# Kernel tuning notes

Hardware: AMD Instinct MI355X
Metric: run time of the kernel (lower is better)

## Reference

```python
import jax, jax.numpy as jnp
import numpy as np

NUM_LAYERS = 2
D_MODEL = 512
NHEAD = 8
SEQ_LEN = 2048
WINDOW = 64
D_FF = 4 * D_MODEL
LN_EPS = 1e-5


def _log_sparse_allowed(seq_len, window_size):
    # True where attention is allowed: causal local window + log2-strided lookback.
    allowed = np.zeros((seq_len, seq_len), dtype=bool)
    for i in range(seq_len):
        allowed[i, max(0, i - window_size): i + 1] = True
        for j in range(int(np.log2(i + 1)) + 1):
            step = 2 ** j
            if i - step >= 0:
                allowed[i, i - step] = True
    return allowed


def setup_inputs() -> dict:
    key = jax.random.key(0)
    ks = jax.random.split(key, 16)
    B = 4
    s = 0.02
    L, D, F = NUM_LAYERS, D_MODEL, D_FF
    inp = {
        "src": jax.random.normal(ks[0], (B, SEQ_LEN, D), dtype=jnp.float32),
        "mask": jnp.asarray(_log_sparse_allowed(SEQ_LEN, WINDOW)),
        "qkv_w": jax.random.normal(ks[1], (L, 3 * D, D), jnp.float32) * s,
        "qkv_b": jnp.zeros((L, 3 * D), jnp.float32),
        "out_w": jax.random.normal(ks[2], (L, D, D), jnp.float32) * s,
        "out_b": jnp.zeros((L, D), jnp.float32),
        "ln1_s": jnp.ones((L, D), jnp.float32),
        "ln1_b": jnp.zeros((L, D), jnp.float32),
        "w1": jax.random.normal(ks[3], (L, F, D), jnp.float32) * s,
        "b1": jnp.zeros((L, F), jnp.float32),
        "w2": jax.random.normal(ks[4], (L, D, F), jnp.float32) * s,
        "b2": jnp.zeros((L, D), jnp.float32),
        "ln2_s": jnp.ones((L, D), jnp.float32),
        "ln2_b": jnp.zeros((L, D), jnp.float32),
    }
    return inp


def _ln(x, scale, bias):
    m = jnp.mean(x, axis=-1, keepdims=True)
    v = jnp.var(x, axis=-1, keepdims=True)
    return (x - m) * jax.lax.rsqrt(v + LN_EPS) * scale + bias


def _encoder(src, mask, qkv_w, qkv_b, out_w, out_b, ln1_s, ln1_b, w1, b1, w2, b2, ln2_s, ln2_b):
    B, S, D = src.shape
    H, dh = NHEAD, D // NHEAD
    x = src
    for l in range(NUM_LAYERS):
        qkv = x @ qkv_w[l].T + qkv_b[l]                       # [B,S,3D]
        q, k, v = jnp.split(qkv, 3, axis=-1)
        q = q.reshape(B, S, H, dh).transpose(0, 2, 1, 3)       # [B,H,S,dh]
        k = k.reshape(B, S, H, dh).transpose(0, 2, 1, 3)
        v = v.reshape(B, S, H, dh).transpose(0, 2, 1, 3)
        scores = jnp.einsum('bhqd,bhkd->bhqk', q, k) / jnp.sqrt(jnp.asarray(dh, x.dtype))
        scores = jnp.where(mask, scores, -jnp.inf)             # additive log-sparse mask
        attn = jax.nn.softmax(scores, axis=-1)
        o = jnp.einsum('bhqk,bhkd->bhqd', attn, v)
        o = o.transpose(0, 2, 1, 3).reshape(B, S, D)
        o = o @ out_w[l].T + out_b[l]
        x = _ln(x + o, ln1_s[l], ln1_b[l])                     # post-norm (norm_first=False)
        h = jax.nn.relu(x @ w1[l].T + b1[l]) @ w2[l].T + b2[l]
        x = _ln(x + h, ln2_s[l], ln2_b[l])
    return x


def reference(src, mask, qkv_w, qkv_b, out_w, out_b, ln1_s, ln1_b, w1, b1, w2, b2, ln2_s, ln2_b):
    return _encoder(src, mask, qkv_w, qkv_b, out_w, out_b, ln1_s, ln1_b, w1, b1, w2, b2, ln2_s, ln2_b)
```

## Files before the change

kernel.cpp:

```cpp
#include <hip/hip_runtime.h>
#include <hip/hip_bf16.h>
#include <cstdint>
#include <cstddef>

using bf16 = __hip_bfloat16;

typedef __attribute__((ext_vector_type(8))) short short8;
typedef __attribute__((ext_vector_type(4))) float floatx4;

constexpr int NLAYERS = 2;
constexpr int D_MODEL = 512;
constexpr int NHEAD   = 8;
constexpr int DH      = 64;
constexpr int SEQ     = 2048;
constexpr int BATCH   = 4;
constexpr int D_FF    = 2048;
constexpr int ROWS    = BATCH * SEQ;

#define MODE_QKV   0
#define MODE_RELU  1
#define MODE_PLAIN 2

constexpr int BN = 128, BK = 64;

union S8 { short8 v; bf16 b[8]; ushort u[8]; };

__device__ inline ushort4 pack4_bf16(float4 v) {
    ushort4 u;
    u.x = __bfloat16_as_ushort(__float2bfloat16(v.x));
    u.y = __bfloat16_as_ushort(__float2bfloat16(v.y));
    u.z = __bfloat16_as_ushort(__float2bfloat16(v.z));
    u.w = __bfloat16_as_ushort(__float2bfloat16(v.w));
    return u;
}

__device__ inline void gld16(const void* g, void* l) {
    __builtin_amdgcn_global_load_lds(
        (const __attribute__((address_space(1))) void*)(uintptr_t)g,
        (__attribute__((address_space(3))) void*)(uint32_t)(uintptr_t)l,
        16, 0, 0);
}

constexpr int CN1 = NLAYERS * 3 * D_MODEL * D_MODEL;
constexpr int CN2 = NLAYERS * D_MODEL * D_MODEL;
constexpr int CN3 = NLAYERS * D_FF * D_MODEL;
constexpr int CN4 = NLAYERS * D_MODEL * D_FF;
constexpr int CN5 = ROWS * D_MODEL;
constexpr int CNT = CN1 + CN2 + CN3 + CN4 + CN5;

__global__ __launch_bounds__(256) void cvt_all(
    const float* __restrict__ a1, const float* __restrict__ a2,
    const float* __restrict__ a3, const float* __restrict__ a4,
    const float* __restrict__ a5,
    bf16* __restrict__ d1, bf16* __restrict__ d2, bf16* __restrict__ d3,
    bf16* __restrict__ d4, bf16* __restrict__ d5)
{
    const int i = (blockIdx.x * 256 + threadIdx.x) * 4;
    const float* s; bf16* d; int off;
    if      (i < CN1)                   { s = a1; d = d1; off = i; }
    else if (i < CN1+CN2)               { s = a2; d = d2; off = i - CN1; }
    else if (i < CN1+CN2+CN3)           { s = a3; d = d3; off = i - (CN1+CN2); }
    else if (i < CN1+CN2+CN3+CN4)       { s = a4; d = d4; off = i - (CN1+CN2+CN3); }
    else if (i < CNT)                   { s = a5; d = d5; off = i - (CN1+CN2+CN3+CN4); }
    else return;
    *(ushort4*)(d + off) = pack4_bf16(*(const float4*)(s + off));
}

template<int TBM>
__global__ __launch_bounds__(256) void gemm_bt(
    const bf16* __restrict__ Ab,
    const bf16* __restrict__ Bw, const float* __restrict__ bias,
    bf16* __restrict__ Cb,
    bf16* __restrict__ Qo, bf16* __restrict__ Ko, bf16* __restrict__ Vo,
    int M, int N, int K, int mode)
{
    constexpr int NJ = (TBM == 128) ? 4 : 2;
    __shared__ bf16 As[2][TBM][BK];
    __shared__ bf16 Bs[2][BN][BK];
    const int tid  = threadIdx.x;
    const int bn   = blockIdx.x * BN;
    const int bm   = blockIdx.y * TBM;
    const int lane = tid & 63;
    const int wave = tid >> 6;
    const int wm   = (TBM == 128) ? (wave & 1) * 64 : 0;
    const int wn   = (TBM == 128) ? (wave >> 1) * 64 : wave * 32;

    floatx4 acc[4][NJ];
    #pragma unroll
    for (int i = 0; i < 4; i++)
        #pragma unroll
        for (int j = 0; j < NJ; j++)
            acc[i][j] = (floatx4){0.f, 0.f, 0.f, 0.f};

    const int l8  = lane >> 3;
    const int c8s = (((lane & 7) ^ l8) * 8);

    auto stage = [&](int buf, int k0) {
        #pragma unroll
        for (int c = 0; c < TBM / 32; ++c) {
            const int rowb = wave * (TBM / 4) + c * 8;
            gld16(Ab + (size_t)(bm + rowb + l8) * K + k0 + c8s, &As[buf][rowb][0]);
        }
        #pragma unroll
        for (int c = 0; c < 4; ++c) {
            const int rowb = wave * 32 + c * 8;
            gld16(Bw + (size_t)(bn + rowb + l8) * K + k0 + c8s, &Bs[buf][rowb][0]);
        }
    };

    const int nt = K / BK;
    stage(0, 0);
    __syncthreads();
    int cur = 0;
    for (int t = 0; t < nt; ++t) {
        if (t + 1 < nt) stage(cur ^ 1, (t + 1) * BK);
        #pragma unroll
        for (int ks = 0; ks < BK; ks += 32) {
            const int kk = ks + (lane >> 4) * 8;
            const int ri = lane & 15;
            const int csw = (((kk >> 3) ^ (ri & 7)) << 3);
            short8 af[4], bfr[NJ];
            #pragma unroll
            for (int i = 0; i < 4; i++) af[i]  = *(const short8*)&As[cur][wm + i*16 + ri][csw];
            #pragma unroll
            for (int j = 0; j < NJ; j++) bfr[j] = *(const short8*)&Bs[cur][wn + j*16 + ri][csw];
            #pragma unroll
            for (int i = 0; i < 4; i++)
                #pragma unroll
                for (int j = 0; j < NJ; j++)
                    acc[i][j] = __builtin_amdgcn_mfma_f32_16x16x32_bf16(af[i], bfr[j], acc[i][j], 0, 0, 0);
        }
        __syncthreads();
        cur ^= 1;
    }

    const int cn = lane & 15;
    const int rb = (lane >> 4) * 4;
    #pragma unroll
    for (int j = 0; j < NJ; j++) {
        const int col = bn + wn + j * 16 + cn;
        const float bv = bias[col];
        #pragma unroll
        for (int i = 0; i < 4; i++) {
            const int row0 = bm + wm + i * 16 + rb;
            if (mode == MODE_RELU) {
                #pragma unroll
                for (int r = 0; r < 4; r++)
                    Cb[(size_t)(row0 + r) * N + col] =
                        __float2bfloat16(fmaxf(acc[i][j][r] + bv, 0.f));
            } else if (mode == MODE_PLAIN) {
                #pragma unroll
                for (int r = 0; r < 4; r++)
                    Cb[(size_t)(row0 + r) * N + col] =
                        __float2bfloat16(acc[i][j][r] + bv);
            } else {
                const int which = col >> 9;
                const int f = col & 511;
                const int h = f >> 6, d = f & 63;
                const int b = row0 >> 11, s = row0 & (SEQ - 1);
                if (which == 2) {
                    ushort4 u;
                    u.x = __bfloat16_as_ushort(__float2bfloat16(acc[i][j][0] + bv));
                    u.y = __bfloat16_as_ushort(__float2bfloat16(acc[i][j][1] + bv));
                    u.z = __bfloat16_as_ushort(__float2bfloat16(acc[i][j][2] + bv));
                    u.w = __bfloat16_as_ushort(__float2bfloat16(acc[i][j][3] + bv));
                    *(ushort4*)(Vo + ((size_t)(b * NHEAD + h) * DH + d) * SEQ + s) = u;
                } else {
                    bf16* dst = (which == 0) ? Qo : Ko;
                    #pragma unroll
                    for (int r = 0; r < 4; r++)
                        dst[(((size_t)b * NHEAD + h) * SEQ + s + r) * DH + d] =
                            __float2bfloat16(acc[i][j][r] + bv);
                }
            }
        }
    }
}

__global__ __launch_bounds__(256, 4) void attn_mfma(
    const bf16* __restrict__ Q, const bf16* __restrict__ K,
    const bf16* __restrict__ Vt, bf16* __restrict__ O)
{
    __shared__ float SL[16][148];
    __shared__ bf16  PL[16][168];
    const int tid  = threadIdx.x;
    const int wave = tid >> 6;
    const int lane = tid & 63;
    const int gq0  = blockIdx.x * 16;
    const int s0   = gq0 & (SEQ - 1);
    const int bh   = gq0 >> 11;

    const bf16* Qb  = Q  + (size_t)bh * SEQ * DH;
    const bf16* Kb  = K  + (size_t)bh * SEQ * DH;
    const bf16* Vtb = Vt + (size_t)bh * DH * SEQ;

    PL[tid >> 4][144 + (tid & 15)] = __float2bfloat16(0.f);

    const int kk = (lane >> 4) * 8;
    const int ri = lane & 15;
    const int cn = lane & 15;
    const int rb = (lane >> 4) * 4;

    {
        short8 a0 = *(const short8*)(Qb + (size_t)(s0 + ri) * DH + kk);
        short8 a1 = *(const short8*)(Qb + (size_t)(s0 + ri) * DH + kk + 32);
        for (int t = wave; t < 9; t += 4) {
            const int r = t * 16 + ri;
            int g;
            if (r < 80) g = s0 - 64 + r;
            else { const int e = r - 80; g = s0 + (e & 15) - (128 << (e >> 4)); }
            g = g < 0 ? 0 : g;
            const bf16* kr = Kb + (size_t)g * DH;
            short8 b0 = *(const short8*)(kr + kk);
            short8 b1 = *(const short8*)(kr + kk + 32);
            floatx4 acc = (floatx4){0.f, 0.f, 0.f, 0.f};
            acc = __builtin_amdgcn_mfma_f32_16x16x32_bf16(a0, b0, acc, 0, 0, 0);
            acc = __builtin_amdgcn_mfma_f32_16x16x32_bf16(a1, b1, acc, 0, 0, 0);
            #pragma unroll
            for (int r2 = 0; r2 < 4; r2++)
                SL[rb + r2][t * 16 + cn] = acc[r2] * 0.125f;
        }
    }
    __syncthreads();

    #pragma unroll
    for (int q4 = 0; q4 < 4; q4++) {
        const int q = wave * 4 + q4;
        const int s = s0 + q;
        float sc[3];
        bool  val[3];
        #pragma unroll
        for (int u = 0; u < 3; u++) {
            const int slot = lane + 64 * u;
            bool v = false;
            if (slot < 144) {
                if (slot < 80) {
                    const int g = s0 - 64 + slot;
                    v = (g >= 0) && (slot >= q) && (slot <= q + 64);
                } else {
                    const int e = slot - 80;
                    v = ((e & 15) == q) && (s - (128 << (e >> 4)) >= 0);
                }
            }
            val[u] = v;
            sc[u] = v ? SL[q][slot] : -1e30f;
        }
        float m = fmaxf(sc[0], fmaxf(sc[1], sc[2]));
        #pragma unroll
        for (int off = 32; off; off >>= 1) m = fmaxf(m, __shfl_xor(m, off, 64));
        float pv[3];
        float lsum = 0.f;
        #pragma unroll
        for (int u = 0; u < 3; u++) {
            pv[u] = val[u] ? __expf(fminf(sc[u] - m, 0.f)) : 0.f;
            lsum += pv[u];
        }
        #pragma unroll
        for (int off = 32; off; off >>= 1) lsum += __shfl_xor(lsum, off, 64);
        const float inv = 1.f / fmaxf(lsum, 1e-20f);
        #pragma unroll
        for (int u = 0; u < 3; u++) {
            const int slot = lane + 64 * u;
            if (slot < 144) PL[q][slot] = __float2bfloat16(pv[u] * inv);
        }
    }
    __syncthreads();

    {
        const int d = wave * 16 + ri;
        const bf16* Vr = Vtb + (size_t)d * SEQ;
        short8 vb[5];
        #pragma unroll
        for (int u = 0; u < 5; u++) {
            const int slot = u * 32 + kk;
            if (slot >= 144) {
                vb[u] = (short8){0, 0, 0, 0, 0, 0, 0, 0};
            } else {
                int g0;
                if (slot < 80) g0 = s0 - 64 + slot;
                else { const int e = slot - 80; g0 = s0 + (e & 15) - (128 << (e >> 4)); }
                g0 = g0 < 0 ? 0 : g0;
                vb[u] = *(const short8*)(Vr + g0);
            }
        }
        floatx4 acc = (floatx4){0.f, 0.f, 0.f, 0.f};
        #pragma unroll
        for (int u = 0; u < 5; u++) {
            short8 a = *(const short8*)&PL[ri][u * 32 + kk];
            acc = __builtin_amdgcn_mfma_f32_16x16x32_bf16(a, vb[u], acc, 0, 0, 0);
        }
        const int b = bh >> 3, h = bh & 7;
        #pragma unroll
        for (int r2 = 0; r2 < 4; r2++)
            O[((size_t)(b * SEQ + s0 + rb + r2)) * D_MODEL + h * DH + wave * 16 + cn]
                = __float2bfloat16(acc[r2]);
    }
}

__global__ __launch_bounds__(256) void ln_residual(
    const bf16* __restrict__ xin_b, const float* __restrict__ xin_f,
    const bf16* __restrict__ t,
    const float* __restrict__ gamma, const float* __restrict__ beta,
    bf16* __restrict__ xout_b, float* __restrict__ xout_f)
{
    const int wave = threadIdx.x >> 6;
    const int lane = threadIdx.x & 63;
    const int row  = blockIdx.x * 4 + wave;
    const size_t base = (size_t)row * D_MODEL + lane * 8;

    float v[8];
    if (xin_f != nullptr) {
        float4 x0 = *(const float4*)(xin_f + base);
        float4 x1 = *(const float4*)(xin_f + base + 4);
        v[0] = x0.x; v[1] = x0.y; v[2] = x0.z; v[3] = x0.w;
        v[4] = x1.x; v[5] = x1.y; v[6] = x1.z; v[7] = x1.w;
    } else {
        S8 xb; xb.v = *(const short8*)(xin_b + base);
        #pragma unroll
        for (int j = 0; j < 8; j++) v[j] = __bfloat162float(xb.b[j]);
    }
    S8 tb; tb.v = *(const short8*)(t + base);
    float sum = 0.f, sq = 0.f;
    #pragma unroll
    for (int j = 0; j < 8; j++) {
        v[j] += __bfloat162float(tb.b[j]);
        sum += v[j];
        sq  += v[j] * v[j];
    }
    #pragma unroll
    for (int off = 32; off; off >>= 1) {
        sum += __shfl_xor(sum, off, 64);
        sq  += __shfl_xor(sq,  off, 64);
    }
    const float mean = sum * (1.f / D_MODEL);
    const float var  = fmaxf(sq * (1.f / D_MODEL) - mean * mean, 0.f);
    const float r    = rsqrtf(var + 1e-5f);
    float4 g0 = *(const float4*)(gamma + lane * 8);
    float4 g1 = *(const float4*)(gamma + lane * 8 + 4);
    float4 b0 = *(const float4*)(beta  + lane * 8);
    float4 b1 = *(const float4*)(beta  + lane * 8 + 4);
    float g[8] = {g0.x, g0.y, g0.z, g0.w, g1.x, g1.y, g1.z, g1.w};
    float bb[8] = {b0.x, b0.y, b0.z, b0.w, b1.x, b1.y, b1.z, b1.w};
    float o[8];
    #pragma unroll
    for (int j = 0; j < 8; j++) o[j] = (v[j] - mean) * r * g[j] + bb[j];
    if (xout_f != nullptr) {
        *(float4*)(xout_f + base)     = (float4){o[0], o[1], o[2], o[3]};
        *(float4*)(xout_f + base + 4) = (float4){o[4], o[5], o[6], o[7]};
    } else {
        S8 ob;
        #pragma unroll
        for (int j = 0; j < 8; j++) ob.b[j] = __float2bfloat16(o[j]);
        *(short8*)(xout_b + base) = ob.v;
    }
}

extern "C" void kernel_launch(void* const* d_in, const int* in_sizes, int n_in,
                              void* d_out, int out_size, void* d_ws, size_t ws_size,
                              hipStream_t stream)
{
    const int want[12] = {1572864, 3072, 524288, 1024, 1024, 1024,
                          2097152, 4096, 2097152, 1024, 1024, 1024};
    int anchor = -1;
    for (int a = 2; a >= 1; --a) {
        if (n_in < a + 12) continue;
        bool ok = true;
        for (int i = 0; i < 12; i++) if (in_sizes[a + i] != want[i]) { ok = false; break; }
        if (ok) { anchor = a; break; }
    }
    if (anchor < 0) return;

    const float* src   = (const float*)d_in[0];
    const float* qkv_w = (const float*)d_in[anchor + 0];
    const float* qkv_b = (const float*)d_in[anchor + 1];
    const float* out_w = (const float*)d_in[anchor + 2];
    const float* out_b = (const float*)d_in[anchor + 3];
    const float* ln1_s = (const float*)d_in[anchor + 4];
    const float* ln1_b = (const float*)d_in[anchor + 5];
    const float* w1    = (const float*)d_in[anchor + 6];
    const float* b1    = (const float*)d_in[anchor + 7];
    const float* w2    = (const float*)d_in[anchor + 8];
    const float* b2    = (const float*)d_in[anchor + 9];
    const float* ln2_s = (const float*)d_in[anchor + 10];
    const float* ln2_b = (const float*)d_in[anchor + 11];
    float* out = (float*)d_out;

    constexpr size_t MiB = 1024 * 1024;
    if (ws_size < 96 * MiB) return;
    char* p = (char*)d_ws;
    bf16*  Q   = (bf16*)(p);
    bf16*  Kt  = (bf16*)(p + 8 * MiB);
    bf16*  Vt  = (bf16*)(p + 16 * MiB);
    bf16*  O   = (bf16*)(p + 24 * MiB);
    bf16*  Hb  = (bf16*)(p);
    bf16*  Tb  = (bf16*)(p + 32 * MiB);
    bf16*  srcB= (bf16*)(p + 40 * MiB);
    bf16*  xA  = (bf16*)(p + 48 * MiB);
    bf16*  qwB = (bf16*)(p + 56 * MiB);
    bf16*  owB = (bf16*)(p + 59 * MiB);
    bf16*  w1B = (bf16*)(p + 60 * MiB);
    bf16*  w2B = (bf16*)(p + 64 * MiB);

    cvt_all<<<dim3(CNT / 4 / 256), 256, 0, stream>>>(
        qkv_w, out_w, w1, w2, src, qwB, owB, w1B, w2B, srcB);

    for (int l = 0; l < NLAYERS; ++l) {
        const bf16*  xin = (l == 0) ? srcB : xA;
        const float* xf  = (l == 0) ? src : nullptr;
        gemm_bt<128><<<dim3((3 * D_MODEL) / BN, ROWS / 128), 256, 0, stream>>>(
            xin, qwB + (size_t)l * 3 * D_MODEL * D_MODEL, qkv_b + (size_t)l * 3 * D_MODEL,
            nullptr, Q, Kt, Vt, ROWS, 3 * D_MODEL, D_MODEL, MODE_QKV);
        attn_mfma<<<dim3(BATCH * NHEAD * SEQ / 16), 256, 0, stream>>>(Q, Kt, Vt, O);
        gemm_bt<64><<<dim3(D_MODEL / BN, ROWS / 64), 256, 0, stream>>>(
            O, owB + (size_t)l * D_MODEL * D_MODEL, out_b + (size_t)l * D_MODEL,
            Tb, nullptr, nullptr, nullptr, ROWS, D_MODEL, D_MODEL, MODE_PLAIN);
        ln_residual<<<dim3(ROWS / 4), 256, 0, stream>>>(
            (l == 0) ? nullptr : xA, xf, Tb,
            ln1_s + (size_t)l * D_MODEL, ln1_b + (size_t)l * D_MODEL,
            xA, nullptr);
        gemm_bt<128><<<dim3(D_FF / BN, ROWS / 128), 256, 0, stream>>>(
            xA, w1B + (size_t)l * D_FF * D_MODEL, b1 + (size_t)l * D_FF,
            Hb, nullptr, nullptr, nullptr, ROWS, D_FF, D_MODEL, MODE_RELU);
        gemm_bt<64><<<dim3(D_MODEL / BN, ROWS / 64), 256, 0, stream>>>(
            Hb, w2B + (size_t)l * D_MODEL * D_FF, b2 + (size_t)l * D_MODEL,
            Tb, nullptr, nullptr, nullptr, ROWS, D_MODEL, D_FF, MODE_PLAIN);
        if (l == NLAYERS - 1) {
            ln_residual<<<dim3(ROWS / 4), 256, 0, stream>>>(
                xA, nullptr, Tb, ln2_s + (size_t)l * D_MODEL, ln2_b + (size_t)l * D_MODEL,
                nullptr, out);
        } else {
            ln_residual<<<dim3(ROWS / 4), 256, 0, stream>>>(
                xA, nullptr, Tb, ln2_s + (size_t)l * D_MODEL, ln2_b + (size_t)l * D_MODEL,
                xA, nullptr);
        }
    }
}
```

Baseline: 405.6 us.

## Split-K the N=512 GEMMs in two and reduce partials inside the LayerNorm kernel

The out-projection and FFN-down GEMMs are launched with a z dimension of 2, and each z-slice computes half of the K reduction. Each slice writes fp32 partial sums to a workspace buffer, with the bias added only by z=0. The LayerNorm-residual kernel now reads both fp32 partials and adds them, so no separate reduction kernel is needed. This doubles the block count for these narrow-N GEMMs, which had only 512 blocks, to improve occupancy across the CUs. The cost is extra fp32 write and read traffic, 2x4 bytes per element instead of 2 bytes, plus a larger workspace.

```diff
diff --git a/kernel.cpp b/kernel.cpp
--- a/kernel.cpp
+++ b/kernel.cpp
@@ -17,9 +17,9 @@
 constexpr int D_FF    = 2048;
 constexpr int ROWS    = BATCH * SEQ;
 
-#define MODE_QKV   0
-#define MODE_RELU  1
-#define MODE_PLAIN 2
+#define MODE_QKV     0
+#define MODE_RELU    1
+#define MODE_PARTIAL 2
 
 constexpr int BN = 128, BK = 64;
 
@@ -70,9 +70,9 @@
 __global__ __launch_bounds__(256) void gemm_bt(
     const bf16* __restrict__ Ab,
     const bf16* __restrict__ Bw, const float* __restrict__ bias,
-    bf16* __restrict__ Cb,
+    bf16* __restrict__ Cb, float* __restrict__ Pp,
     bf16* __restrict__ Qo, bf16* __restrict__ Ko, bf16* __restrict__ Vo,
-    int M, int N, int K, int mode)
+    int M, int N, int Kfull, int Ksub, int mode)
 {
     constexpr int NJ = (TBM == 128) ? 4 : 2;
     __shared__ bf16 As[2][TBM][BK];
@@ -80,6 +80,9 @@
     const int tid  = threadIdx.x;
     const int bn   = blockIdx.x * BN;
     const int bm   = blockIdx.y * TBM;
+    const int z    = blockIdx.z;
+    const int koff = z * Ksub;
+    const int K    = Kfull;
     const int lane = tid & 63;
     const int wave = tid >> 6;
     const int wm   = (TBM == 128) ? (wave & 1) * 64 : 0;
@@ -108,12 +111,12 @@
         }
     };
 
-    const int nt = K / BK;
-    stage(0, 0);
+    const int nt = Ksub / BK;
+    stage(0, koff);
     __syncthreads();
     int cur = 0;
     for (int t = 0; t < nt; ++t) {
-        if (t + 1 < nt) stage(cur ^ 1, (t + 1) * BK);
+        if (t + 1 < nt) stage(cur ^ 1, koff + (t + 1) * BK);
         #pragma unroll
         for (int ks = 0; ks < BK; ks += 32) {
             const int kk = ks + (lane >> 4) * 8;
@@ -139,20 +142,20 @@
     #pragma unroll
     for (int j = 0; j < NJ; j++) {
         const int col = bn + wn + j * 16 + cn;
-        const float bv = bias[col];
+        const float bv = (mode == MODE_PARTIAL && z != 0) ? 0.f : bias[col];
         #pragma unroll
         for (int i = 0; i < 4; i++) {
             const int row0 = bm + wm + i * 16 + rb;
-            if (mode == MODE_RELU) {
+            if (mode == MODE_PARTIAL) {
+                float* dst = Pp + (size_t)z * M * N;
+                #pragma unroll
+                for (int r = 0; r < 4; r++)
+                    dst[(size_t)(row0 + r) * N + col] = acc[i][j][r] + bv;
+            } else if (mode == MODE_RELU) {
                 #pragma unroll
                 for (int r = 0; r < 4; r++)
                     Cb[(size_t)(row0 + r) * N + col] =
                         __float2bfloat16(fmaxf(acc[i][j][r] + bv, 0.f));
-            } else if (mode == MODE_PLAIN) {
-                #pragma unroll
-                for (int r = 0; r < 4; r++)
-                    Cb[(size_t)(row0 + r) * N + col] =
-                        __float2bfloat16(acc[i][j][r] + bv);
             } else {
                 const int which = col >> 9;
                 const int f = col & 511;
@@ -299,7 +302,7 @@
 
 __global__ __launch_bounds__(256) void ln_residual(
     const bf16* __restrict__ xin_b, const float* __restrict__ xin_f,
-    const bf16* __restrict__ t,
+    const float* __restrict__ p0, const float* __restrict__ p1,
     const float* __restrict__ gamma, const float* __restrict__ beta,
     bf16* __restrict__ xout_b, float* __restrict__ xout_f)
 {
@@ -319,11 +322,16 @@
         #pragma unroll
         for (int j = 0; j < 8; j++) v[j] = __bfloat162float(xb.b[j]);
     }
-    S8 tb; tb.v = *(const short8*)(t + base);
+    float4 pa0 = *(const float4*)(p0 + base);
+    float4 pa1 = *(const float4*)(p0 + base + 4);
+    float4 pb0 = *(const float4*)(p1 + base);
+    float4 pb1 = *(const float4*)(p1 + base + 4);
+    float p[8] = {pa0.x + pb0.x, pa0.y + pb0.y, pa0.z + pb0.z, pa0.w + pb0.w,
+                  pa1.x + pb1.x, pa1.y + pb1.y, pa1.z + pb1.z, pa1.w + pb1.w};
     float sum = 0.f, sq = 0.f;
     #pragma unroll
     for (int j = 0; j < 8; j++) {
-        v[j] += __bfloat162float(tb.b[j]);
+        v[j] += p[j];
         sum += v[j];
         sq  += v[j] * v[j];
     }
@@ -386,20 +394,22 @@
     float* out = (float*)d_out;
 
     constexpr size_t MiB = 1024 * 1024;
-    if (ws_size < 96 * MiB) return;
+    if (ws_size < 104 * MiB) return;
     char* p = (char*)d_ws;
     bf16*  Q   = (bf16*)(p);
     bf16*  Kt  = (bf16*)(p + 8 * MiB);
     bf16*  Vt  = (bf16*)(p + 16 * MiB);
     bf16*  O   = (bf16*)(p + 24 * MiB);
     bf16*  Hb  = (bf16*)(p);
-    bf16*  Tb  = (bf16*)(p + 32 * MiB);
-    bf16*  srcB= (bf16*)(p + 40 * MiB);
-    bf16*  xA  = (bf16*)(p + 48 * MiB);
-    bf16*  qwB = (bf16*)(p + 56 * MiB);
-    bf16*  owB = (bf16*)(p + 59 * MiB);
-    bf16*  w1B = (bf16*)(p + 60 * MiB);
-    bf16*  w2B = (bf16*)(p + 64 * MiB);
+    float* P01 = (float*)(p + 32 * MiB);
+    float* P   = P01;
+    bf16*  srcB= (bf16*)(p + 64 * MiB);
+    bf16*  xA  = (bf16*)(p + 72 * MiB);
+    bf16*  qwB = (bf16*)(p + 80 * MiB);
+    bf16*  owB = (bf16*)(p + 83 * MiB);
+    bf16*  w1B = (bf16*)(p + 84 * MiB);
+    bf16*  w2B = (bf16*)(p + 88 * MiB);
+    float* P1  = P + (size_t)ROWS * D_MODEL;
 
     cvt_all<<<dim3(CNT / 4 / 256), 256, 0, stream>>>(
         qkv_w, out_w, w1, w2, src, qwB, owB, w1B, w2B, srcB);
@@ -407,30 +417,33 @@
     for (int l = 0; l < NLAYERS; ++l) {
         const bf16*  xin = (l == 0) ? srcB : xA;
         const float* xf  = (l == 0) ? src : nullptr;
-        gemm_bt<128><<<dim3((3 * D_MODEL) / BN, ROWS / 128), 256, 0, stream>>>(
+        gemm_bt<128><<<dim3((3 * D_MODEL) / BN, ROWS / 128, 1), 256, 0, stream>>>(
             xin, qwB + (size_t)l * 3 * D_MODEL * D_MODEL, qkv_b + (size_t)l * 3 * D_MODEL,
-            nullptr, Q, Kt, Vt, ROWS, 3 * D_MODEL, D_MODEL, MODE_QKV);
+            nullptr, nullptr, Q, Kt, Vt, ROWS, 3 * D_MODEL, D_MODEL, D_MODEL, MODE_QKV);
         attn_mfma<<<dim3(BATCH * NHEAD * SEQ / 16), 256, 0, stream>>>(Q, Kt, Vt, O);
-        gemm_bt<64><<<dim3(D_MODEL / BN, ROWS / 64), 256, 0, stream>>>(
+        gemm_bt<64><<<dim3(D_MODEL / BN, ROWS / 64, 2), 256, 0, stream>>>(
             O, owB + (size_t)l * D_MODEL * D_MODEL, out_b + (size_t)l * D_MODEL,
-            Tb, nullptr, nullptr, nullptr, ROWS, D_MODEL, D_MODEL, MODE_PLAIN);
+            nullptr, P, nullptr, nullptr, nullptr,
+            ROWS, D_MODEL, D_MODEL, D_MODEL / 2, MODE_PARTIAL);
         ln_residual<<<dim3(ROWS / 4), 256, 0, stream>>>(
-            (l == 0) ? nullptr : xA, xf, Tb,
+            (l == 0) ? nullptr : xA, xf, P, P1,
             ln1_s + (size_t)l * D_MODEL, ln1_b + (size_t)l * D_MODEL,
             xA, nullptr);
-        gemm_bt<128><<<dim3(D_FF / BN, ROWS / 128), 256, 0, stream>>>(
+        gemm_bt<128><<<dim3(D_FF / BN, ROWS / 128, 1), 256, 0, stream>>>(
             xA, w1B + (size_t)l * D_FF * D_MODEL, b1 + (size_t)l * D_FF,
-            Hb, nullptr, nullptr, nullptr, ROWS, D_FF, D_MODEL, MODE_RELU);
-        gemm_bt<64><<<dim3(D_MODEL / BN, ROWS / 64), 256, 0, stream>>>(
+            Hb, nullptr, nullptr, nullptr, nullptr,
+            ROWS, D_FF, D_MODEL, D_MODEL, MODE_RELU);
+        gemm_bt<64><<<dim3(D_MODEL / BN, ROWS / 64, 2), 256, 0, stream>>>(
             Hb, w2B + (size_t)l * D_MODEL * D_FF, b2 + (size_t)l * D_MODEL,
-            Tb, nullptr, nullptr, nullptr, ROWS, D_MODEL, D_FF, MODE_PLAIN);
+            nullptr, P, nullptr, nullptr, nullptr,
+            ROWS, D_MODEL, D_FF, D_FF / 2, MODE_PARTIAL);
         if (l == NLAYERS - 1) {
             ln_residual<<<dim3(ROWS / 4), 256, 0, stream>>>(
-                xA, nullptr, Tb, ln2_s + (size_t)l * D_MODEL, ln2_b + (size_t)l * D_MODEL,
+                xA, nullptr, P, P1, ln2_s + (size_t)l * D_MODEL, ln2_b + (size_t)l * D_MODEL,
                 nullptr, out);
         } else {
             ln_residual<<<dim3(ROWS / 4), 256, 0, stream>>>(
-                xA, nullptr, Tb, ln2_s + (size_t)l * D_MODEL, ln2_b + (size_t)l * D_MODEL,
+                xA, nullptr, P, P1, ln2_s + (size_t)l * D_MODEL, ln2_b + (size_t)l * D_MODEL,
                 xA, nullptr);
         }
     }
```

After: 425.8 us. +5.0%, slower.
